# Performance work log

Hardware: AMD Instinct MI355X
Metric: run time of the kernel (lower is better)

The kernel has to match this reference:

```python
import jax, jax.numpy as jnp
import numpy as np

D_MODEL = 1024
NHEAD = 16
HEAD_DIM = D_MODEL // NHEAD
MLP_DIM = 4096
ROPE_THETA = 10000.0


def layer_norm(x, g, b, eps=1e-5):
    mu = jnp.mean(x, axis=-1, keepdims=True)
    var = jnp.var(x, axis=-1, keepdims=True)
    return (x - mu) * jax.lax.rsqrt(var + eps) * g + b


def rope_cos_sin(seq_len, dim):
    # lucidrains RotaryEmbedding: inv_freq over even indices, freqs repeated interleaved
    inv_freq = 1.0 / (ROPE_THETA ** (jnp.arange(0, dim, 2, dtype=jnp.float32) / dim))
    t = jnp.arange(seq_len, dtype=jnp.float32)
    freqs = t[:, None] * inv_freq[None, :]            # (S, dim/2)
    freqs = jnp.repeat(freqs, 2, axis=-1)             # (S, dim) interleaved [f0,f0,f1,f1,...]
    return jnp.cos(freqs), jnp.sin(freqs)


def apply_rope(x, cos, sin):
    # x: (B, S, H, D); interleaved rotate_half: (x0,x1) -> (-x1, x0)
    x1 = x[..., ::2]
    x2 = x[..., 1::2]
    rot = jnp.stack([-x2, x1], axis=-1).reshape(x.shape)
    c = cos[None, :, None, :]
    s = sin[None, :, None, :]
    return x * c + rot * s


def setup_inputs() -> dict:
    key = jax.random.key(0)
    ks = jax.random.split(key, 8)
    B, S = 2, 2048
    sc = 1.0 / np.sqrt(D_MODEL)
    inputs = jax.random.normal(ks[0], (B, S, D_MODEL), dtype=jnp.float32)
    return {
        "inputs": inputs,
        "ln1_g": jnp.ones((D_MODEL,), jnp.float32),
        "ln1_b": jnp.zeros((D_MODEL,), jnp.float32),
        "Wq": jax.random.normal(ks[1], (D_MODEL, D_MODEL), jnp.float32) * sc,
        "Wk": jax.random.normal(ks[2], (D_MODEL, D_MODEL), jnp.float32) * sc,
        "Wv": jax.random.normal(ks[3], (D_MODEL, D_MODEL), jnp.float32) * sc,
        "Wo": jax.random.normal(ks[4], (D_MODEL, D_MODEL), jnp.float32) * sc,
        "ln2_g": jnp.ones((D_MODEL,), jnp.float32),
        "ln2_b": jnp.zeros((D_MODEL,), jnp.float32),
        "Wfc2": jax.random.normal(ks[5], (D_MODEL, MLP_DIM), jnp.float32) * sc,
        "bfc2": jnp.zeros((MLP_DIM,), jnp.float32),
        "Wfc3": jax.random.normal(ks[6], (MLP_DIM, D_MODEL), jnp.float32) * (1.0 / np.sqrt(MLP_DIM)),
        "bfc3": jnp.zeros((D_MODEL,), jnp.float32),
    }


def reference(inputs, ln1_g, ln1_b, Wq, Wk, Wv, Wo, ln2_g, ln2_b, Wfc2, bfc2, Wfc3, bfc3):
    B, S, _ = inputs.shape
    x = layer_norm(inputs, ln1_g, ln1_b)
    q = (x @ Wq).reshape(B, S, NHEAD, HEAD_DIM)
    k = (x @ Wk).reshape(B, S, NHEAD, HEAD_DIM)
    v = (x @ Wv).reshape(B, S, NHEAD, HEAD_DIM)
    cos, sin = rope_cos_sin(S, HEAD_DIM)
    q = apply_rope(q, cos, sin)
    k = apply_rope(k, cos, sin)
    scores = jnp.einsum('bqhd,bkhd->bhqk', q, k) / np.sqrt(HEAD_DIM)
    attn = jax.nn.softmax(scores, axis=-1)
    out = jnp.einsum('bhqk,bkhd->bqhd', attn, v).reshape(B, S, D_MODEL)
    out = out @ Wo
    mlp_in = out + inputs
    h = layer_norm(mlp_in, ln2_g, ln2_b)
    h = jax.nn.gelu(h @ Wfc2 + bfc2, approximate=False)
    h = h @ Wfc3 + bfc3
    return h + mlp_in
```

## Files before the change

kernel.cpp:

```cpp
#include <hip/hip_runtime.h>
#include <cstdint>
#include <cstddef>

typedef __bf16 bf16x8 __attribute__((ext_vector_type(8)));
typedef __bf16 bf16x4 __attribute__((ext_vector_type(4)));
typedef float  f32x4  __attribute__((ext_vector_type(4)));
typedef float  f32x16 __attribute__((ext_vector_type(16)));

__device__ __forceinline__ void load16_to_lds(const void* g, void* l) {
  __builtin_amdgcn_global_load_lds(
      (const __attribute__((address_space(1))) void*)g,
      (__attribute__((address_space(3))) void*)l, 16, 0, 0);
}

__global__ __launch_bounds__(256) void transpose_cast(
    const float* __restrict__ src, __bf16* __restrict__ dst, int K, int N)
{
  __shared__ float tile[32][33];
  const int n0 = blockIdx.x * 32, k0 = blockIdx.y * 32;
  const int tx = threadIdx.x, ty = threadIdx.y;
#pragma unroll
  for (int i = 0; i < 32; i += 8)
    tile[ty + i][tx] = src[(size_t)(k0 + ty + i) * N + n0 + tx];
  __syncthreads();
#pragma unroll
  for (int i = 0; i < 32; i += 8)
    dst[(size_t)(n0 + ty + i) * K + k0 + tx] = (__bf16)tile[tx][ty + i];
}

__global__ __launch_bounds__(256) void transpose_cast_qkv(
    const float* __restrict__ s0, const float* __restrict__ s1,
    const float* __restrict__ s2, __bf16* __restrict__ dst)
{
  __shared__ float tile[32][33];
  const float* src = blockIdx.z == 0 ? s0 : blockIdx.z == 1 ? s1 : s2;
  __bf16* d = dst + (size_t)blockIdx.z * 1024 * 1024;
  const int n0 = blockIdx.x * 32, k0 = blockIdx.y * 32;
  const int tx = threadIdx.x, ty = threadIdx.y;
#pragma unroll
  for (int i = 0; i < 32; i += 8)
    tile[ty + i][tx] = src[(size_t)(k0 + ty + i) * 1024 + n0 + tx];
  __syncthreads();
#pragma unroll
  for (int i = 0; i < 32; i += 8)
    d[(size_t)(n0 + ty + i) * 1024 + k0 + tx] = (__bf16)tile[tx][ty + i];
}

__global__ __launch_bounds__(256) void ln_kernel(
    const float* __restrict__ x, const float* __restrict__ g,
    const float* __restrict__ bta, __bf16* __restrict__ out)
{
  const int row = blockIdx.x;
  const int t = threadIdx.x;
  const float4 v = ((const float4*)(x + (size_t)row * 1024))[t];
  float s  = v.x + v.y + v.z + v.w;
  float ss = v.x * v.x + v.y * v.y + v.z * v.z + v.w * v.w;
#pragma unroll
  for (int o = 32; o > 0; o >>= 1) { s += __shfl_down(s, o); ss += __shfl_down(ss, o); }
  __shared__ float rs[4], rss[4];
  const int w = t >> 6, l = t & 63;
  if (l == 0) { rs[w] = s; rss[w] = ss; }
  __syncthreads();
  s  = rs[0] + rs[1] + rs[2] + rs[3];
  ss = rss[0] + rss[1] + rss[2] + rss[3];
  const float mu = s * (1.0f / 1024.0f);
  const float var = ss * (1.0f / 1024.0f) - mu * mu;
  const float rstd = rsqrtf(var + 1e-5f);
  const float4 gg = ((const float4*)g)[t];
  const float4 bb = ((const float4*)bta)[t];
  __bf16* o = out + (size_t)row * 1024 + t * 4;
  o[0] = (__bf16)((v.x - mu) * rstd * gg.x + bb.x);
  o[1] = (__bf16)((v.y - mu) * rstd * gg.y + bb.y);
  o[2] = (__bf16)((v.z - mu) * rstd * gg.z + bb.z);
  o[3] = (__bf16)((v.w - mu) * rstd * gg.w + bb.w);
}

enum { EPI_BF16 = 0, EPI_RES_F32 = 1, EPI_GELU_BF16 = 2, EPI_BIAS_RES_F32 = 3 };

template <int TM, int EPI>
__global__ __launch_bounds__(256, 2) void gemm_bf16(
    const __bf16* __restrict__ A, const __bf16* __restrict__ Bt,
    __bf16* __restrict__ outb, float* __restrict__ outf,
    const float* __restrict__ bias, const float* __restrict__ res,
    int M, int N, int K)
{
  constexpr int MT = TM / 32;
  __shared__ __bf16 As[2][TM * 32];
  __shared__ __bf16 Bs[2][128 * 32];
  const int tid  = threadIdx.x;
  const int lane = tid & 63, w = tid >> 6;
  const int wm = w >> 1, wn = w & 1;
  const int quad = lane >> 4, l16 = lane & 15;
  const int m0 = blockIdx.y * TM, n0 = blockIdx.x * 128;

  f32x4 acc[MT][4] = {};
  const __bf16* Ag = A  + (size_t)m0 * K;
  const __bf16* Bg = Bt + (size_t)n0 * K;

#pragma unroll
  for (int r = 0; r < TM / 64; ++r) {
    const int c = r * 256 + tid;
    const int row = c >> 2, cc = (c & 3) * 8;
    load16_to_lds(Ag + (size_t)row * K + cc, &As[0][c * 8]);
  }
#pragma unroll
  for (int r = 0; r < 2; ++r) {
    const int c = r * 256 + tid;
    const int row = c >> 2, cc = (c & 3) * 8;
    load16_to_lds(Bg + (size_t)row * K + cc, &Bs[0][c * 8]);
  }

  const int nk = K >> 5;
  for (int kt = 0; kt < nk; ++kt) {
    __syncthreads();
    const int p = kt & 1;

    if (kt + 1 < nk) {
      const int k1 = (kt + 1) * 32;
#pragma unroll
      for (int r = 0; r < TM / 64; ++r) {
        const int c = r * 256 + tid;
        const int row = c >> 2, cc = (c & 3) * 8;
        load16_to_lds(Ag + (size_t)row * K + k1 + cc, &As[1 - p][c * 8]);
      }
#pragma unroll
      for (int r = 0; r < 2; ++r) {
        const int c = r * 256 + tid;
        const int row = c >> 2, cc = (c & 3) * 8;
        load16_to_lds(Bg + (size_t)row * K + k1 + cc, &Bs[1 - p][c * 8]);
      }
    }

    bf16x8 af[MT], bfr[4];
#pragma unroll
    for (int mt = 0; mt < MT; ++mt)
      af[mt] = *(const bf16x8*)&As[p][(wm * (TM / 2) + mt * 16 + l16) * 32 + quad * 8];
#pragma unroll
    for (int nt = 0; nt < 4; ++nt)
      bfr[nt] = *(const bf16x8*)&Bs[p][(wn * 64 + nt * 16 + l16) * 32 + quad * 8];

#pragma unroll
    for (int mt = 0; mt < MT; ++mt)
#pragma unroll
      for (int nt = 0; nt < 4; ++nt)
        acc[mt][nt] = __builtin_amdgcn_mfma_f32_16x16x32_bf16(af[mt], bfr[nt], acc[mt][nt], 0, 0, 0);
  }

#pragma unroll
  for (int mt = 0; mt < MT; ++mt) {
#pragma unroll
    for (int nt = 0; nt < 4; ++nt) {
      const int col = n0 + wn * 64 + nt * 16 + l16;
#pragma unroll
      for (int i = 0; i < 4; ++i) {
        const int row = m0 + wm * (TM / 2) + mt * 16 + quad * 4 + i;
        float v = acc[mt][nt][i];
        const size_t idx = (size_t)row * N + col;
        if (EPI == EPI_BF16) {
          outb[idx] = (__bf16)v;
        } else if (EPI == EPI_RES_F32) {
          outf[idx] = v + res[idx];
        } else if (EPI == EPI_GELU_BF16) {
          v += bias[col];
          outb[idx] = (__bf16)(0.5f * v * (1.0f + erff(v * 0.70710678118f)));
        } else {
          v += bias[col];
          outf[idx] = v + res[idx];
        }
      }
    }
  }
}

__global__ __launch_bounds__(256) void rope_qk(
    const __bf16* __restrict__ qkv, __bf16* __restrict__ qr, __bf16* __restrict__ kr)
{
  const int idx = blockIdx.x * 256 + threadIdx.x;
  const int d2 = idx & 31;
  const int h  = (idx >> 5) & 15;
  const int bs = idx >> 9;
  const int s  = bs & 2047;
  const int b  = bs >> 11;
  const float inv_freq = exp2f(-((float)d2 * (1.0f / 32.0f)) * 13.2877123795f);
  const float ang = (float)s * inv_freq;
  const float c = cosf(ang), sn = sinf(ang);
  const float QS = 0.125f * 1.44269504f;
  const __bf16* qp = qkv + (size_t)bs * 3072 + h * 64 + 2 * d2;
  const __bf16* kp = qp + 1024;
  const float q0 = (float)qp[0], q1 = (float)qp[1];
  const float k0 = (float)kp[0], k1 = (float)kp[1];
  const size_t o = ((size_t)(b * 16 + h) * 2048 + s) * 64 + 2 * d2;
  qr[o]     = (__bf16)((q0 * c - q1 * sn) * QS);
  qr[o + 1] = (__bf16)((q1 * c + q0 * sn) * QS);
  kr[o]     = (__bf16)(k0 * c - k1 * sn);
  kr[o + 1] = (__bf16)(k1 * c + k0 * sn);
}

__global__ __launch_bounds__(256) void v_transpose(
    const __bf16* __restrict__ qkv, __bf16* __restrict__ vt)
{
  __shared__ __bf16 t[64][72];
  const int st = blockIdx.x, h = blockIdx.y, b = blockIdx.z;
  const int tx = threadIdx.x & 63, ty = threadIdx.x >> 6;
  const int s0 = st * 64;
  const __bf16* src = qkv + ((size_t)(b * 2048 + s0)) * 3072 + 2048 + h * 64;
#pragma unroll
  for (int i = 0; i < 64; i += 4)
    t[ty + i][tx] = src[(size_t)(ty + i) * 3072 + tx];
  __syncthreads();
  __bf16* dst = vt + ((size_t)(b * 16 + h) * 64) * 2048 + s0;
#pragma unroll
  for (int i = 0; i < 64; i += 4)
    dst[(size_t)(ty + i) * 2048 + tx] = t[tx][ty + i];
}

__global__ __launch_bounds__(256, 2) void attn_kernel(
    const __bf16* __restrict__ qr, const __bf16* __restrict__ kr,
    const __bf16* __restrict__ vt, __bf16* __restrict__ attn_o)
{
  constexpr int S = 2048, DH = 64, NH = 16, BQ = 128, BKK = 64;
  __shared__ __align__(16) __bf16 smem[24576];
  __bf16* Qs   = smem;
  __bf16* Ksb  = smem + 8192;
  __bf16* Vtsb = smem + 16384;

  const int tid = threadIdx.x;
  const int lane = tid & 63, w = tid >> 6;
  const int l32 = lane & 31, half = lane >> 5;
  const int qt = blockIdx.x, h = blockIdx.y, b = blockIdx.z;
  const int bh = b * NH + h;
  const __bf16* Q  = qr + ((size_t)bh * S + qt * BQ) * DH;
  const __bf16* Kp = kr + (size_t)bh * S * DH;
  const __bf16* Vp = vt + (size_t)bh * DH * S;
  __bf16* Pb = Qs + w * 2048;

#pragma unroll
  for (int r4 = 0; r4 < 4; ++r4) {
    const int c = r4 * 256 + tid;
    const int r = c >> 3, cb = c & 7;
    load16_to_lds(Q + (size_t)r * DH + ((cb ^ (r & 7)) * 8), &Qs[c * 8]);
  }
#pragma unroll
  for (int r2 = 0; r2 < 2; ++r2) {
    const int c = r2 * 256 + tid;
    const int r = c >> 3, cb = c & 7;
    const int cg = (cb ^ (r & 7)) * 8;
    load16_to_lds(Kp + (size_t)r * DH + cg, &Ksb[c * 8]);
    load16_to_lds(Vp + (size_t)r * S + cg, &Vtsb[c * 8]);
  }
  __syncthreads();

  bf16x8 qfB[4];
  {
    const int row = w * 32 + l32;
#pragma unroll
    for (int c = 0; c < 4; ++c)
      qfB[c] = *(const bf16x8*)&Qs[row * 64 + (((2 * c + half) ^ (row & 7)) * 8)];
  }

  float mreg = -3.0e38f, lreg = 0.0f;
  f32x16 oacc[2] = {};

  for (int kt = 0; kt < S / BKK; ++kt) {
    if (kt) __syncthreads();

    if (kt + 1 < S / BKK) {
      __bf16* Kn = Ksb  + ((kt + 1) & 1) * 4096;
      __bf16* Vn = Vtsb + ((kt + 1) & 1) * 4096;
      const size_t kk1 = (size_t)(kt + 1) * BKK;
#pragma unroll
      for (int r2 = 0; r2 < 2; ++r2) {
        const int c = r2 * 256 + tid;
        const int r = c >> 3, cb = c & 7;
        const int cg = (cb ^ (r & 7)) * 8;
        load16_to_lds(Kp + (kk1 + r) * DH + cg, &Kn[c * 8]);
        load16_to_lds(Vp + (size_t)r * S + kk1 + cg, &Vn[c * 8]);
      }
    }

    const __bf16* Ks  = Ksb  + (kt & 1) * 4096;
    const __bf16* Vts = Vtsb + (kt & 1) * 4096;

    bf16x8 kf[2][4], vf[2][4];
#pragma unroll
    for (int t = 0; t < 2; ++t) {
      const int row = 32 * t + l32;
#pragma unroll
      for (int c = 0; c < 4; ++c)
        kf[t][c] = *(const bf16x8*)&Ks[row * 64 + (((2 * c + half) ^ (l32 & 7)) * 8)];
    }
#pragma unroll
    for (int v = 0; v < 2; ++v) {
      const int row = 32 * v + l32;
#pragma unroll
      for (int c = 0; c < 4; ++c)
        vf[v][c] = *(const bf16x8*)&Vts[row * 64 + (((2 * c + half) ^ (l32 & 7)) * 8)];
    }

    f32x16 sa[2] = {};
#pragma unroll
    for (int t = 0; t < 2; ++t)
#pragma unroll
      for (int c = 0; c < 4; ++c)
        sa[t] = __builtin_amdgcn_mfma_f32_32x32x16_bf16(kf[t][c], qfB[c], sa[t], 0, 0, 0);

    float mx = -3.0e38f;
#pragma unroll
    for (int t = 0; t < 2; ++t)
#pragma unroll
      for (int r = 0; r < 16; ++r) mx = fmaxf(mx, sa[t][r]);
    mx = fmaxf(mx, __shfl_xor(mx, 32));
    const float mnew = fmaxf(mreg, mx);
    const float alpha = exp2f(mreg - mnew);
    mreg = mnew;
    float sum = 0.0f;
#pragma unroll
    for (int t = 0; t < 2; ++t)
#pragma unroll
      for (int r = 0; r < 16; ++r) {
        const float p = exp2f(sa[t][r] - mnew);
        sa[t][r] = p;
        sum += p;
      }
    sum += __shfl_xor(sum, 32);
    lreg = lreg * alpha + sum;
#pragma unroll
    for (int v = 0; v < 2; ++v)
#pragma unroll
      for (int r = 0; r < 16; ++r) oacc[v][r] *= alpha;

#pragma unroll
    for (int t = 0; t < 2; ++t)
#pragma unroll
      for (int g = 0; g < 4; ++g) {
        bf16x4 pv;
#pragma unroll
        for (int i = 0; i < 4; ++i) pv[i] = (__bf16)sa[t][4 * g + i];
        const int kc = 4 * t + g;
        *(bf16x4*)&Pb[l32 * 64 + ((kc ^ (l32 & 7)) * 8) + 4 * half] = pv;
      }

    bf16x8 pf[4];
#pragma unroll
    for (int c = 0; c < 4; ++c)
      pf[c] = *(const bf16x8*)&Pb[l32 * 64 + (((2 * c + half) ^ (l32 & 7)) * 8)];
#pragma unroll
    for (int v = 0; v < 2; ++v)
#pragma unroll
      for (int c = 0; c < 4; ++c)
        oacc[v] = __builtin_amdgcn_mfma_f32_32x32x16_bf16(vf[v][c], pf[c], oacc[v], 0, 0, 0);
  }

  const float linv = 1.0f / lreg;
#pragma unroll
  for (int v = 0; v < 2; ++v)
#pragma unroll
    for (int g = 0; g < 4; ++g) {
      bf16x4 ov;
#pragma unroll
      for (int i = 0; i < 4; ++i) ov[i] = (__bf16)(oacc[v][4 * g + i] * linv);
      const int dc = 4 * v + g;
      *(bf16x4*)&Pb[l32 * 64 + ((dc ^ (l32 & 7)) * 8) + 4 * half] = ov;
    }
#pragma unroll
  for (int cc = 0; cc < 4; ++cc) {
    const int c = cc * 64 + lane;
    const int r = c >> 3, g = c & 7;
    const bf16x8 od = *(const bf16x8*)&Pb[r * 64 + ((g ^ (r & 7)) * 8)];
    const int srow = qt * BQ + w * 32 + r;
    *(bf16x8*)&attn_o[((size_t)b * S + srow) * 1024 + h * 64 + g * 8] = od;
  }
}

extern "C" void kernel_launch(void* const* d_in, const int* in_sizes, int n_in,
                              void* d_out, int out_size, void* d_ws, size_t ws_size,
                              hipStream_t stream) {
  const float* inputs = (const float*)d_in[0];
  const float* ln1_g  = (const float*)d_in[1];
  const float* ln1_b  = (const float*)d_in[2];
  const float* Wq     = (const float*)d_in[3];
  const float* Wk     = (const float*)d_in[4];
  const float* Wv     = (const float*)d_in[5];
  const float* Wo     = (const float*)d_in[6];
  const float* ln2_g  = (const float*)d_in[7];
  const float* ln2_b  = (const float*)d_in[8];
  const float* Wfc2   = (const float*)d_in[9];
  const float* bfc2   = (const float*)d_in[10];
  const float* Wfc3   = (const float*)d_in[11];
  const float* bfc3   = (const float*)d_in[12];
  float* out = (float*)d_out;
  char* ws = (char*)d_ws;
  const size_t MB = 1024 * 1024;

  __bf16* Wqkv_t = (__bf16*)(ws);
  __bf16* Wo_t   = (__bf16*)(ws + 6 * MB);
  __bf16* Wfc2_t = (__bf16*)(ws + 8 * MB);
  __bf16* Wfc3_t = (__bf16*)(ws + 16 * MB);
  __bf16* xb     = (__bf16*)(ws + 24 * MB);
  __bf16* attn_o = xb;
  __bf16* qkv    = (__bf16*)(ws + 32 * MB);
  float*  mlp_in = (float*)(ws + 32 * MB);
  __bf16* h2     = (__bf16*)(ws + 48 * MB);
  __bf16* qrb    = (__bf16*)(ws + 56 * MB);
  __bf16* krb    = (__bf16*)(ws + 64 * MB);
  __bf16* vtb    = (__bf16*)(ws + 72 * MB);
  __bf16* hbuf   = (__bf16*)(ws + 56 * MB);

  const dim3 tb(32, 8);
  transpose_cast_qkv<<<dim3(32, 32, 3), tb, 0, stream>>>(Wq, Wk, Wv, Wqkv_t);
  transpose_cast<<<dim3(32, 32),  tb, 0, stream>>>(Wo,   Wo_t,   1024, 1024);
  transpose_cast<<<dim3(128, 32), tb, 0, stream>>>(Wfc2, Wfc2_t, 1024, 4096);
  transpose_cast<<<dim3(32, 128), tb, 0, stream>>>(Wfc3, Wfc3_t, 4096, 1024);

  ln_kernel<<<4096, 256, 0, stream>>>(inputs, ln1_g, ln1_b, xb);

  gemm_bf16<64, EPI_BF16><<<dim3(24, 64), 256, 0, stream>>>(
      xb, Wqkv_t, qkv, nullptr, nullptr, nullptr, 4096, 3072, 1024);

  rope_qk<<<8192, 256, 0, stream>>>(qkv, qrb, krb);
  v_transpose<<<dim3(32, 16, 2), 256, 0, stream>>>(qkv, vtb);

  attn_kernel<<<dim3(16, 16, 2), 256, 0, stream>>>(qrb, krb, vtb, attn_o);

  gemm_bf16<64, EPI_RES_F32><<<dim3(8, 64), 256, 0, stream>>>(
      attn_o, Wo_t, nullptr, mlp_in, nullptr, inputs, 4096, 1024, 1024);

  ln_kernel<<<4096, 256, 0, stream>>>(mlp_in, ln2_g, ln2_b, h2);

  gemm_bf16<128, EPI_GELU_BF16><<<dim3(32, 32), 256, 0, stream>>>(
      h2, Wfc2_t, hbuf, nullptr, bfc2, nullptr, 4096, 4096, 1024);

  gemm_bf16<64, EPI_BIAS_RES_F32><<<dim3(8, 64), 256, 0, stream>>>(
      hbuf, Wfc3_t, nullptr, out, bfc3, mlp_in, 4096, 1024, 4096);
}
```

Measured before the change: 403.8 us.

## Add K-depth template with swizzled LDS tiles and hoist fragment loads before prefetch

The GEMM gains a template parameter for the K tile depth. The Wo and Wfc3 GEMMs now use a 64-deep K tile with an XOR-swizzled LDS layout, which halves the number of barriers per K and avoids bank conflicts. In both the GEMM and the attention kernel, fragments are read from LDS before the next tile's async global-to-LDS prefetch is issued, which is meant to improve overlap. The larger tiles use more LDS, which may cut occupancy for those kernels.

```diff
diff --git a/kernel.cpp b/kernel.cpp
--- a/kernel.cpp
+++ b/kernel.cpp
@@ -77,7 +77,7 @@
 
 enum { EPI_BF16 = 0, EPI_RES_F32 = 1, EPI_GELU_BF16 = 2, EPI_BIAS_RES_F32 = 3 };
 
-template <int TM, int EPI>
+template <int TM, int KB, int EPI>
 __global__ __launch_bounds__(256, 2) void gemm_bf16(
     const __bf16* __restrict__ A, const __bf16* __restrict__ Bt,
     __bf16* __restrict__ outb, float* __restrict__ outf,
@@ -85,8 +85,9 @@
     int M, int N, int K)
 {
   constexpr int MT = TM / 32;
-  __shared__ __bf16 As[2][TM * 32];
-  __shared__ __bf16 Bs[2][128 * 32];
+  constexpr int KS = KB / 32;
+  __shared__ __bf16 As[2][TM * KB];
+  __shared__ __bf16 Bs[2][128 * KB];
   const int tid  = threadIdx.x;
   const int lane = tid & 63, w = tid >> 6;
   const int wm = w >> 1, wn = w & 1;
@@ -97,53 +98,66 @@
   const __bf16* Ag = A  + (size_t)m0 * K;
   const __bf16* Bg = Bt + (size_t)n0 * K;
 
-#pragma unroll
-  for (int r = 0; r < TM / 64; ++r) {
-    const int c = r * 256 + tid;
-    const int row = c >> 2, cc = (c & 3) * 8;
-    load16_to_lds(Ag + (size_t)row * K + cc, &As[0][c * 8]);
-  }
-#pragma unroll
-  for (int r = 0; r < 2; ++r) {
-    const int c = r * 256 + tid;
-    const int row = c >> 2, cc = (c & 3) * 8;
-    load16_to_lds(Bg + (size_t)row * K + cc, &Bs[0][c * 8]);
-  }
-
-  const int nk = K >> 5;
+  auto stageA = [&](int buf, int k0) {
+#pragma unroll
+    for (int r2 = 0; r2 < TM * KB / 8 / 256; ++r2) {
+      const int c = r2 * 256 + tid;
+      const int r = c / (KB / 8), cb = c % (KB / 8);
+      const int g = (KB == 64) ? (cb ^ (r & 7)) : cb;
+      load16_to_lds(Ag + (size_t)r * K + k0 + g * 8, &As[buf][c * 8]);
+    }
+  };
+  auto stageB = [&](int buf, int k0) {
+#pragma unroll
+    for (int r2 = 0; r2 < 128 * KB / 8 / 256; ++r2) {
+      const int c = r2 * 256 + tid;
+      const int r = c / (KB / 8), cb = c % (KB / 8);
+      const int g = (KB == 64) ? (cb ^ (r & 7)) : cb;
+      load16_to_lds(Bg + (size_t)r * K + k0 + g * 8, &Bs[buf][c * 8]);
+    }
+  };
+
+  stageA(0, 0);
+  stageB(0, 0);
+
+  const int nk = K / KB;
   for (int kt = 0; kt < nk; ++kt) {
     __syncthreads();
     const int p = kt & 1;
 
+    bf16x8 af[MT][KS], bfr[4][KS];
+#pragma unroll
+    for (int mt = 0; mt < MT; ++mt) {
+      const int row = wm * (TM / 2) + mt * 16 + l16;
+#pragma unroll
+      for (int ks = 0; ks < KS; ++ks) {
+        const int ch = (KB == 64) ? ((ks * 4 + quad) ^ (row & 7)) : quad;
+        af[mt][ks] = *(const bf16x8*)&As[p][row * KB + ch * 8];
+      }
+    }
+#pragma unroll
+    for (int nt = 0; nt < 4; ++nt) {
+      const int row = wn * 64 + nt * 16 + l16;
+#pragma unroll
+      for (int ks = 0; ks < KS; ++ks) {
+        const int ch = (KB == 64) ? ((ks * 4 + quad) ^ (row & 7)) : quad;
+        bfr[nt][ks] = *(const bf16x8*)&Bs[p][row * KB + ch * 8];
+      }
+    }
+
     if (kt + 1 < nk) {
-      const int k1 = (kt + 1) * 32;
-#pragma unroll
-      for (int r = 0; r < TM / 64; ++r) {
-        const int c = r * 256 + tid;
-        const int row = c >> 2, cc = (c & 3) * 8;
-        load16_to_lds(Ag + (size_t)row * K + k1 + cc, &As[1 - p][c * 8]);
-      }
-#pragma unroll
-      for (int r = 0; r < 2; ++r) {
-        const int c = r * 256 + tid;
-        const int row = c >> 2, cc = (c & 3) * 8;
-        load16_to_lds(Bg + (size_t)row * K + k1 + cc, &Bs[1 - p][c * 8]);
-      }
-    }
-
-    bf16x8 af[MT], bfr[4];
-#pragma unroll
-    for (int mt = 0; mt < MT; ++mt)
-      af[mt] = *(const bf16x8*)&As[p][(wm * (TM / 2) + mt * 16 + l16) * 32 + quad * 8];
-#pragma unroll
-    for (int nt = 0; nt < 4; ++nt)
-      bfr[nt] = *(const bf16x8*)&Bs[p][(wn * 64 + nt * 16 + l16) * 32 + quad * 8];
-
-#pragma unroll
-    for (int mt = 0; mt < MT; ++mt)
-#pragma unroll
-      for (int nt = 0; nt < 4; ++nt)
-        acc[mt][nt] = __builtin_amdgcn_mfma_f32_16x16x32_bf16(af[mt], bfr[nt], acc[mt][nt], 0, 0, 0);
+      stageA(1 - p, (kt + 1) * KB);
+      stageB(1 - p, (kt + 1) * KB);
+    }
+
+#pragma unroll
+    for (int ks = 0; ks < KS; ++ks)
+#pragma unroll
+      for (int mt = 0; mt < MT; ++mt)
+#pragma unroll
+        for (int nt = 0; nt < 4; ++nt)
+          acc[mt][nt] = __builtin_amdgcn_mfma_f32_16x16x32_bf16(
+              af[mt][ks], bfr[nt][ks], acc[mt][nt], 0, 0, 0);
   }
 
 #pragma unroll
@@ -263,6 +277,24 @@
 
   for (int kt = 0; kt < S / BKK; ++kt) {
     if (kt) __syncthreads();
+    const __bf16* Ks  = Ksb  + (kt & 1) * 4096;
+    const __bf16* Vts = Vtsb + (kt & 1) * 4096;
+
+    bf16x8 kf[2][4], vf[2][4];
+#pragma unroll
+    for (int t = 0; t < 2; ++t) {
+      const int row = 32 * t + l32;
+#pragma unroll
+      for (int c = 0; c < 4; ++c)
+        kf[t][c] = *(const bf16x8*)&Ks[row * 64 + (((2 * c + half) ^ (l32 & 7)) * 8)];
+    }
+#pragma unroll
+    for (int v = 0; v < 2; ++v) {
+      const int row = 32 * v + l32;
+#pragma unroll
+      for (int c = 0; c < 4; ++c)
+        vf[v][c] = *(const bf16x8*)&Vts[row * 64 + (((2 * c + half) ^ (l32 & 7)) * 8)];
+    }
 
     if (kt + 1 < S / BKK) {
       __bf16* Kn = Ksb  + ((kt + 1) & 1) * 4096;
@@ -276,25 +308,6 @@
         load16_to_lds(Kp + (kk1 + r) * DH + cg, &Kn[c * 8]);
         load16_to_lds(Vp + (size_t)r * S + kk1 + cg, &Vn[c * 8]);
       }
-    }
-
-    const __bf16* Ks  = Ksb  + (kt & 1) * 4096;
-    const __bf16* Vts = Vtsb + (kt & 1) * 4096;
-
-    bf16x8 kf[2][4], vf[2][4];
-#pragma unroll
-    for (int t = 0; t < 2; ++t) {
-      const int row = 32 * t + l32;
-#pragma unroll
-      for (int c = 0; c < 4; ++c)
-        kf[t][c] = *(const bf16x8*)&Ks[row * 64 + (((2 * c + half) ^ (l32 & 7)) * 8)];
-    }
-#pragma unroll
-    for (int v = 0; v < 2; ++v) {
-      const int row = 32 * v + l32;
-#pragma unroll
-      for (int c = 0; c < 4; ++c)
-        vf[v][c] = *(const bf16x8*)&Vts[row * 64 + (((2 * c + half) ^ (l32 & 7)) * 8)];
     }
 
     f32x16 sa[2] = {};
@@ -414,7 +427,7 @@
 
   ln_kernel<<<4096, 256, 0, stream>>>(inputs, ln1_g, ln1_b, xb);
 
-  gemm_bf16<64, EPI_BF16><<<dim3(24, 64), 256, 0, stream>>>(
+  gemm_bf16<64, 32, EPI_BF16><<<dim3(24, 64), 256, 0, stream>>>(
       xb, Wqkv_t, qkv, nullptr, nullptr, nullptr, 4096, 3072, 1024);
 
   rope_qk<<<8192, 256, 0, stream>>>(qkv, qrb, krb);
@@ -422,14 +435,14 @@
 
   attn_kernel<<<dim3(16, 16, 2), 256, 0, stream>>>(qrb, krb, vtb, attn_o);
 
-  gemm_bf16<64, EPI_RES_F32><<<dim3(8, 64), 256, 0, stream>>>(
+  gemm_bf16<64, 64, EPI_RES_F32><<<dim3(8, 64), 256, 0, stream>>>(
       attn_o, Wo_t, nullptr, mlp_in, nullptr, inputs, 4096, 1024, 1024);
 
   ln_kernel<<<4096, 256, 0, stream>>>(mlp_in, ln2_g, ln2_b, h2);
 
-  gemm_bf16<128, EPI_GELU_BF16><<<dim3(32, 32), 256, 0, stream>>>(
+  gemm_bf16<128, 32, EPI_GELU_BF16><<<dim3(32, 32), 256, 0, stream>>>(
       h2, Wfc2_t, hbuf, nullptr, bfc2, nullptr, 4096, 4096, 1024);
 
-  gemm_bf16<64, EPI_BIAS_RES_F32><<<dim3(8, 64), 256, 0, stream>>>(
+  gemm_bf16<64, 64, EPI_BIAS_RES_F32><<<dim3(8, 64), 256, 0, stream>>>(
       hbuf, Wfc3_t, nullptr, out, bfc3, mlp_in, 4096, 1024, 4096);
 }
```

Result: faster. 387.0 us (-4.1%).
